# Performance work log

Hardware: AMD Instinct MI355X
Metric: run time of the kernel (lower is better)

## Reference

```python
import jax, jax.numpy as jnp
import numpy as np
import math

B, L, D = 4, 2048, 768
N_HEADS = 12
CHUNK = 8  # query_mask=1 every CHUNK tokens -> f = B*L/CHUNK, f % B == 0
VOCAB = 50000


def setup_inputs() -> dict:
    key = jax.random.key(0)
    ks = jax.random.split(key, 8)
    scale = 1.0 / math.sqrt(D)
    x_qk = jax.random.normal(ks[0], (B, L, D), jnp.float32)
    x_v = jax.random.normal(ks[1], (B, L, D), jnp.float32)
    # deterministic query mask: feature boundary every CHUNK tokens
    pos = jnp.arange(L)
    query_mask = jnp.tile((pos % CHUNK == 0).astype(jnp.int32)[None, :], (B, 1))
    input_ids = jax.random.randint(ks[2], (B, L), 2, VOCAB).astype(jnp.int64)
    # make the last 16 tokens of each row padding to exercise the pad mask
    input_ids = input_ids.at[:, -16:].set(1)
    Wq = jax.random.normal(ks[3], (D, D), jnp.float32) * scale
    Wk = jax.random.normal(ks[4], (D, D), jnp.float32) * scale
    Wv = jax.random.normal(ks[5], (D, D), jnp.float32) * scale
    Wo = jax.random.normal(ks[6], (D, D), jnp.float32) * scale
    zb = jnp.zeros((D,), jnp.float32)
    return {"x_qk": x_qk, "x_v": x_v, "query_mask": query_mask,
            "input_ids": input_ids, "pad_token_id": 1,
            "Wq": Wq, "bq": zb, "Wk": Wk, "bk": zb,
            "Wv": Wv, "bv": zb, "Wo": Wo, "bo": zb}


def reference(x_qk, x_v, query_mask, input_ids, pad_token_id,
              Wq, bq, Wk, bk, Wv, bv, Wo, bo):
    b, l, d = x_qk.shape
    n = b * l
    qm = query_mask.reshape(-1)
    f = int(np.asarray(jnp.sum(qm)))  # static feature count (f % b == 0)
    idx = jnp.nonzero(qm == 1, size=f)[0]                     # [f] query positions
    # segment boundaries: [left_i, right_i) per feature
    left = idx
    right = jnp.concatenate([idx[1:], jnp.array([n], idx.dtype)])
    pos = jnp.arange(n)
    seg_mask = (pos[None, :] >= left[:, None]) & (pos[None, :] < right[:, None])
    seg_mask = seg_mask & (input_ids.reshape(-1) != pad_token_id)[None, :]  # [f, n]

    xq = x_qk.reshape(n, d)
    xv = x_v.reshape(n, d)
    query = xq[idx]                                           # [f, d]
    q = query @ Wq.T + bq                                     # [f, d]
    k = xq @ Wk.T + bk                                        # [n, d]
    v = xv @ Wv.T + bv                                        # [n, d]

    dh = d // N_HEADS
    qh = q.reshape(f, N_HEADS, dh).transpose(1, 0, 2)         # [h, f, dh]
    kh = k.reshape(n, N_HEADS, dh).transpose(1, 0, 2)         # [h, n, dh]
    vh = v.reshape(n, N_HEADS, dh).transpose(1, 0, 2)         # [h, n, dh]

    bias = (1.0 - seg_mask.astype(jnp.float32)) * -10000.0    # [f, n]
    scores = jnp.einsum('hfd,hnd->hfn', qh, kh) / math.sqrt(dh) + bias[None]
    attn = jax.nn.softmax(scores, axis=-1)                    # [h, f, n]
    out = jnp.einsum('hfn,hnd->hfd', attn, vh)                # [h, f, dh]
    out = out.transpose(1, 0, 2).reshape(f, d)
    out = out @ Wo.T + bo
    return out.reshape(b, f // b, d)
```

## Files before the change

### kernel.cpp

```cpp
#include <hip/hip_runtime.h>

#define DMODEL 768
#define NHEADS 12
#define MAXFULL 16

typedef __attribute__((ext_vector_type(8))) short short8;
typedef __attribute__((ext_vector_type(4))) float f32x4;

__device__ __forceinline__ unsigned pack2_bf16(float a, float b) {
  unsigned ua = __float_as_uint(a), ub = __float_as_uint(b);
  ua = (ua + 0x7fffu + ((ua >> 16) & 1u)) >> 16;
  ub = (ub + 0x7fffu + ((ub >> 16) & 1u)) & 0xffff0000u;
  return ua | ub;
}
__device__ __forceinline__ unsigned short bf16_1(float a) {
  unsigned ua = __float_as_uint(a);
  return (unsigned short)((ua + 0x7fffu + ((ua >> 16) & 1u)) >> 16);
}

__device__ __forceinline__ void load16_lds(const void* g, void* l) {
  __builtin_amdgcn_global_load_lds(
      (const __attribute__((address_space(1))) unsigned int*)g,
      (__attribute__((address_space(3))) unsigned int*)l, 16, 0, 0);
}

__global__ __launch_bounds__(256) void convW(const float* __restrict__ w0,
    const float* __restrict__ w1, const float* __restrict__ w2,
    const float* __restrict__ w3, unsigned* __restrict__ o0,
    unsigned* __restrict__ o1, unsigned* __restrict__ o2,
    unsigned* __restrict__ o3, int count) {
  const int nv = count >> 2;
  const float* src[4] = {w0, w1, w2, w3};
  unsigned* dst[4] = {o0, o1, o2, o3};
  for (int idx = blockIdx.x * 256 + threadIdx.x; idx < 4 * nv;
       idx += gridDim.x * 256) {
    int m = idx / nv, r = idx - m * nv;
    float4 v = ((const float4*)src[m])[r];
    dst[m][2 * r]     = pack2_bf16(v.x, v.y);
    dst[m][2 * r + 1] = pack2_bf16(v.z, v.w);
  }
}

__global__ __launch_bounds__(256) void convX(const float* __restrict__ x0,
    const float* __restrict__ x1, unsigned* __restrict__ o0,
    unsigned* __restrict__ o1, int count) {
  const int nv = count >> 2;
  for (int idx = blockIdx.x * 256 + threadIdx.x; idx < 2 * nv;
       idx += gridDim.x * 256) {
    int m = idx / nv, r = idx - m * nv;
    float4 v = m ? ((const float4*)x1)[r] : ((const float4*)x0)[r];
    unsigned* d = m ? o1 : o0;
    d[2 * r]     = pack2_bf16(v.x, v.y);
    d[2 * r + 1] = pack2_bf16(v.z, v.w);
  }
}

struct GSeg {
  const unsigned short* A;
  const unsigned short* W;
  const float* bias;
  const int* row_map;
  float* C;
  int base;
};

__global__ __launch_bounds__(256) void gemm128(GSeg g0, GSeg g1, GSeg g2) {
  __shared__ __attribute__((aligned(16))) unsigned short As[128 * 32];
  __shared__ __attribute__((aligned(16))) unsigned short Bs[128 * 32];
  const int t = threadIdx.x;
  const int id = blockIdx.x;
  const GSeg& d = (id >= g2.base) ? g2 : ((id >= g1.base) ? g1 : g0);
  const int lid = id - d.base;
  const int xcd = lid & 7, j = lid >> 3;
  const int bn = (j % 6) * 128;
  const int bm = ((j / 6) * 8 + xcd) * 128;
  const int lane = t & 63, wid = t >> 6;
  const int m16 = lane & 15, quad = lane >> 4;
  const int wm = (wid >> 1) * 64, wn = (wid & 1) * 64;

  f32x4 acc[4][4];
#pragma unroll
  for (int i = 0; i < 4; ++i)
#pragma unroll
    for (int j2 = 0; j2 < 4; ++j2) acc[i][j2] = (f32x4){0.f, 0.f, 0.f, 0.f};

  const int srow = wid * 32 + (lane >> 2);
  const int skc = (lane & 3) * 8;
  int arow0, arow1;
  if (d.row_map) {
    arow0 = d.row_map[bm + srow];
    arow1 = d.row_map[bm + srow + 16];
  } else {
    arow0 = bm + srow;
    arow1 = bm + srow + 16;
  }
  const int wrow0 = bn + srow, wrow1 = bn + srow + 16;
  unsigned short* As0 = &As[(wid * 32) * 32];
  unsigned short* As1 = &As[(wid * 32 + 16) * 32];
  unsigned short* Bs0 = &Bs[(wid * 32) * 32];
  unsigned short* Bs1 = &Bs[(wid * 32 + 16) * 32];

  for (int k0 = 0; k0 < DMODEL; k0 += 32) {
    load16_lds(d.A + (size_t)arow0 * DMODEL + k0 + skc, As0);
    load16_lds(d.A + (size_t)arow1 * DMODEL + k0 + skc, As1);
    load16_lds(d.W + (size_t)wrow0 * DMODEL + k0 + skc, Bs0);
    load16_lds(d.W + (size_t)wrow1 * DMODEL + k0 + skc, Bs1);
    __syncthreads();
    short8 a[4], b[4];
#pragma unroll
    for (int i = 0; i < 4; ++i)
      a[i] = *(const short8*)&As[(wm + i * 16 + m16) * 32 + quad * 8];
#pragma unroll
    for (int j2 = 0; j2 < 4; ++j2)
      b[j2] = *(const short8*)&Bs[(wn + j2 * 16 + m16) * 32 + quad * 8];
#pragma unroll
    for (int i = 0; i < 4; ++i)
#pragma unroll
      for (int j2 = 0; j2 < 4; ++j2)
        acc[i][j2] = __builtin_amdgcn_mfma_f32_16x16x32_bf16(a[i], b[j2], acc[i][j2], 0, 0, 0);
    __syncthreads();
  }

  float bv[4]; int bcol[4];
#pragma unroll
  for (int j2 = 0; j2 < 4; ++j2) {
    bcol[j2] = bn + wn + j2 * 16 + m16;
    bv[j2] = d.bias[bcol[j2]];
  }
#pragma unroll
  for (int i = 0; i < 4; ++i) {
    const int rbase = bm + wm + i * 16 + quad * 4;
#pragma unroll
    for (int r = 0; r < 4; ++r) {
      const int row = rbase + r;
#pragma unroll
      for (int j2 = 0; j2 < 4; ++j2)
        d.C[(size_t)row * DMODEL + bcol[j2]] = acc[i][j2][r] + bv[j2];
    }
  }
}

__global__ __launch_bounds__(1024) void build_segments(const int* __restrict__ qm,
    const int* __restrict__ ids, const int* __restrict__ padp,
    int n, int f, int* __restrict__ left, int* __restrict__ right,
    int* __restrict__ nvalid, int* __restrict__ fullrank,
    int* __restrict__ fullist, int* __restrict__ nfull) {
  __shared__ int cnt[1024];
  __shared__ int fullcnt;
  const int t = threadIdx.x;
  if (t == 0) fullcnt = 0;
  const int per = (n + 1023) >> 10;
  const int base = t * per;
  int c = 0;
  for (int i = 0; i < per; ++i) {
    int p = base + i;
    if (p < n && qm[p] != 0) ++c;
  }
  cnt[t] = c;
  __syncthreads();
  for (int off = 1; off < 1024; off <<= 1) {
    int v = (t >= off) ? cnt[t - off] : 0;
    __syncthreads();
    cnt[t] += v;
    __syncthreads();
  }
  int r = cnt[t] - c;
  for (int i = 0; i < per; ++i) {
    int p = base + i;
    if (p < n && qm[p] != 0) {
      if (r < f) left[r] = p;
      ++r;
    }
  }
  __syncthreads();
  const int pad = *padp;
  for (int i = t; i < f; i += 1024) {
    int L0 = left[i];
    int R0 = (i + 1 < f) ? left[i + 1] : n;
    right[i] = R0;
    int cv = 0;
    for (int p = L0; p < R0; ++p) cv += (ids[p] != pad) ? 1 : 0;
    nvalid[i] = cv;
    if (cv == 0) {
      int rk = atomicAdd(&fullcnt, 1);
      if (rk < MAXFULL) { fullist[rk] = i; fullrank[i] = rk; }
      else fullrank[i] = -1;
    } else {
      fullrank[i] = -1;
    }
  }
  __syncthreads();
  if (t == 0) *nfull = (fullcnt < MAXFULL) ? fullcnt : MAXFULL;
}

__device__ __forceinline__ float allreduce64(float x) {
#pragma unroll
  for (int m = 1; m < 64; m <<= 1) x += __shfl_xor(x, m, 64);
  return x;
}

__global__ __launch_bounds__(64) void attn_seg(const float* __restrict__ q,
    const float* __restrict__ k, const float* __restrict__ v,
    const int* __restrict__ left, const int* __restrict__ right,
    const int* __restrict__ nvalid, const int* __restrict__ ids,
    const int* __restrict__ padp, unsigned short* __restrict__ out) {
  const int feat = blockIdx.x, h = blockIdx.y, lane = threadIdx.x;
  if (nvalid[feat] == 0) return;
  const int off = h * 64 + lane;
  const int pad = *padp;
  const float qv = q[(size_t)feat * DMODEL + off];
  float m = -1e30f, l = 0.f, acc = 0.f;
  const int L0 = left[feat], R0 = right[feat];
  for (int p = L0; p < R0; ++p) {
    if (ids[p] == pad) continue;
    float s = allreduce64(qv * k[(size_t)p * DMODEL + off]) * 0.125f;
    float mn = fmaxf(m, s);
    float al = __expf(m - mn);
    float w = __expf(s - mn);
    l = l * al + w;
    acc = acc * al + w * v[(size_t)p * DMODEL + off];
    m = mn;
  }
  out[(size_t)feat * DMODEL + off] = bf16_1(acc / l);
}

__global__ __launch_bounds__(256) void attn_full_part(const float* __restrict__ q,
    const float* __restrict__ k, const float* __restrict__ v,
    const int* __restrict__ fullist, const int* __restrict__ nfullp,
    int n, int P, float* __restrict__ pm, float* __restrict__ pl,
    float* __restrict__ pacc) {
  const int nfull = *nfullp;
  if (nfull == 0) return;
  const int t = threadIdx.x, lane = t & 63, wv = t >> 6;
  const int gw = blockIdx.x * 4 + wv;
  const int h = gw / P, piece = gw - h * P;
  const int pk = n / P;

  __shared__ float q_lds[8 * 64];
  __shared__ float w_lds[4][64 * 8];

  for (int idx = t; idx < 8 * 64; idx += 256) {
    int fl = idx >> 6, d = idx & 63;
    q_lds[idx] = (fl < nfull) ? q[(size_t)fullist[fl] * DMODEL + h * 64 + d] : 0.f;
  }
  __syncthreads();

  float m[8], l[8], acc[8];
#pragma unroll
  for (int f_ = 0; f_ < 8; ++f_) { m[f_] = -1e30f; l[f_] = 0.f; acc[f_] = 0.f; }

  for (int c = 0; c < pk; c += 64) {
    const int pc = piece * pk + c;
    float s[8];
#pragma unroll
    for (int f_ = 0; f_ < 8; ++f_) s[f_] = 0.f;
    const float4* kp = (const float4*)(k + (size_t)(pc + lane) * DMODEL + h * 64);
#pragma unroll 1
    for (int g = 0; g < 2; ++g) {
      float4 kv0 = kp[g * 8 + 0], kv1 = kp[g * 8 + 1], kv2 = kp[g * 8 + 2],
             kv3 = kp[g * 8 + 3], kv4 = kp[g * 8 + 4], kv5 = kp[g * 8 + 5],
             kv6 = kp[g * 8 + 6], kv7 = kp[g * 8 + 7];
      const float4* qb = (const float4*)&q_lds[g * 32];
#pragma unroll
      for (int f_ = 0; f_ < 8; ++f_) {
        float4 q0 = qb[f_ * 16 + 0], q1 = qb[f_ * 16 + 1], q2 = qb[f_ * 16 + 2],
               q3 = qb[f_ * 16 + 3], q4 = qb[f_ * 16 + 4], q5 = qb[f_ * 16 + 5],
               q6 = qb[f_ * 16 + 6], q7 = qb[f_ * 16 + 7];
        float acc0 = q0.x * kv0.x + q0.y * kv0.y + q0.z * kv0.z + q0.w * kv0.w;
        acc0 += q1.x * kv1.x + q1.y * kv1.y + q1.z * kv1.z + q1.w * kv1.w;
        acc0 += q2.x * kv2.x + q2.y * kv2.y + q2.z * kv2.z + q2.w * kv2.w;
        acc0 += q3.x * kv3.x + q3.y * kv3.y + q3.z * kv3.z + q3.w * kv3.w;
        acc0 += q4.x * kv4.x + q4.y * kv4.y + q4.z * kv4.z + q4.w * kv4.w;
        acc0 += q5.x * kv5.x + q5.y * kv5.y + q5.z * kv5.z + q5.w * kv5.w;
        acc0 += q6.x * kv6.x + q6.y * kv6.y + q6.z * kv6.z + q6.w * kv6.w;
        acc0 += q7.x * kv7.x + q7.y * kv7.y + q7.z * kv7.z + q7.w * kv7.w;
        s[f_] += acc0;
      }
    }
    float mx[8];
#pragma unroll
    for (int f_ = 0; f_ < 8; ++f_) mx[f_] = s[f_] * 0.125f;
#pragma unroll
    for (int f_ = 0; f_ < 8; ++f_) s[f_] = mx[f_];
#pragma unroll
    for (int st = 1; st < 64; st <<= 1)
#pragma unroll
      for (int f_ = 0; f_ < 8; ++f_) mx[f_] = fmaxf(mx[f_], __shfl_xor(mx[f_], st, 64));
    float alpha[8], w[8], sum[8];
#pragma unroll
    for (int f_ = 0; f_ < 8; ++f_) {
      float mn = fmaxf(m[f_], mx[f_]);
      alpha[f_] = __expf(m[f_] - mn);
      w[f_] = __expf(s[f_] - mn);
      m[f_] = mn;
      sum[f_] = w[f_];
    }
#pragma unroll
    for (int st = 1; st < 64; st <<= 1)
#pragma unroll
      for (int f_ = 0; f_ < 8; ++f_) sum[f_] += __shfl_xor(sum[f_], st, 64);
#pragma unroll
    for (int f_ = 0; f_ < 8; ++f_) l[f_] = l[f_] * alpha[f_] + sum[f_];
    *(float4*)&w_lds[wv][lane * 8]     = make_float4(w[0], w[1], w[2], w[3]);
    *(float4*)&w_lds[wv][lane * 8 + 4] = make_float4(w[4], w[5], w[6], w[7]);
#pragma unroll
    for (int f_ = 0; f_ < 8; ++f_) acc[f_] *= alpha[f_];
    const float* vb = v + (size_t)pc * DMODEL + h * 64 + lane;
#pragma unroll 4
    for (int kk = 0; kk < 64; ++kk) {
      float vd = vb[(size_t)kk * DMODEL];
      float4 wa = *(const float4*)&w_lds[wv][kk * 8];
      float4 wb = *(const float4*)&w_lds[wv][kk * 8 + 4];
      acc[0] += wa.x * vd; acc[1] += wa.y * vd; acc[2] += wa.z * vd; acc[3] += wa.w * vd;
      acc[4] += wb.x * vd; acc[5] += wb.y * vd; acc[6] += wb.z * vd; acc[7] += wb.w * vd;
    }
  }

  for (int f_ = 0; f_ < nfull; ++f_) {
    size_t idx = ((size_t)f_ * NHEADS + h) * P + piece;
    if (lane == 0) { pm[idx] = m[f_]; pl[idx] = l[f_]; }
    pacc[idx * 64 + lane] = acc[f_];
  }
}

__global__ __launch_bounds__(256) void attn_full_comb(
    const int* __restrict__ fullist, const int* __restrict__ nfullp,
    int P, const float* __restrict__ pm, const float* __restrict__ pl,
    const float* __restrict__ pacc, unsigned short* __restrict__ out) {
  const int fl = blockIdx.x, h = blockIdx.y;
  if (fl >= *nfullp) return;
  const int feat = fullist[fl];
  const int t = threadIdx.x, lane = t & 63, wv = t >> 6;
  const size_t base = ((size_t)fl * NHEADS + h) * P;

  __shared__ float s_pm[128];
  __shared__ float s_sc[128];
  __shared__ float s_red[4];
  __shared__ float s_part[4][64];

  for (int sp = t; sp < P; sp += 256) s_pm[sp] = pm[base + sp];
  __syncthreads();
  float mloc = -1e30f;
  for (int sp = t; sp < P; sp += 256) mloc = fmaxf(mloc, s_pm[sp]);
#pragma unroll
  for (int st = 1; st < 64; st <<= 1) mloc = fmaxf(mloc, __shfl_xor(mloc, st, 64));
  if (lane == 0) s_red[wv] = mloc;
  __syncthreads();
  const float M = fmaxf(fmaxf(s_red[0], s_red[1]), fmaxf(s_red[2], s_red[3]));
  __syncthreads();
  float lloc = 0.f;
  for (int sp = t; sp < P; sp += 256) {
    float sc = __expf(s_pm[sp] - M);
    s_sc[sp] = sc;
    lloc += pl[base + sp] * sc;
  }
#pragma unroll
  for (int st = 1; st < 64; st <<= 1) lloc += __shfl_xor(lloc, st, 64);
  if (lane == 0) s_red[wv] = lloc;
  __syncthreads();
  const float Lt = s_red[0] + s_red[1] + s_red[2] + s_red[3];
  float At = 0.f;
  for (int sp = wv; sp < P; sp += 4)
    At += pacc[(base + sp) * 64 + lane] * s_sc[sp];
  s_part[wv][lane] = At;
  __syncthreads();
  if (wv == 0) {
    float tot = s_part[0][lane] + s_part[1][lane] + s_part[2][lane] + s_part[3][lane];
    out[(size_t)feat * DMODEL + h * 64 + lane] = bf16_1(tot / Lt);
  }
}

extern "C" void kernel_launch(void* const* d_in, const int* in_sizes, int n_in,
                              void* d_out, int out_size, void* d_ws, size_t ws_size,
                              hipStream_t stream) {
  const float* x_qk = (const float*)d_in[0];
  const float* x_v  = (const float*)d_in[1];
  const int* qm     = (const int*)d_in[2];
  const int* ids    = (const int*)d_in[3];
  const int* padp   = (const int*)d_in[4];
  const float* Wq = (const float*)d_in[5];
  const float* bq = (const float*)d_in[6];
  const float* Wk = (const float*)d_in[7];
  const float* bk = (const float*)d_in[8];
  const float* Wv = (const float*)d_in[9];
  const float* bv = (const float*)d_in[10];
  const float* Wo = (const float*)d_in[11];
  const float* bo = (const float*)d_in[12];

  const int n = in_sizes[0] / DMODEL;
  const int f = out_size / DMODEL;

  float* kf = (float*)d_ws;
  float* vf = kf + (size_t)n * DMODEL;
  float* qf = vf + (size_t)n * DMODEL;
  unsigned short* af = (unsigned short*)(qf + (size_t)f * DMODEL);
  unsigned short* wqb = af + (size_t)f * DMODEL;
  unsigned short* wkb = wqb + DMODEL * DMODEL;
  unsigned short* wvb = wkb + DMODEL * DMODEL;
  unsigned short* wob = wvb + DMODEL * DMODEL;
  unsigned short* xqb = wob + DMODEL * DMODEL;
  unsigned short* xvb = xqb + (size_t)n * DMODEL;
  int* left     = (int*)(xvb + (size_t)n * DMODEL);
  int* right    = left + f;
  int* nvalid   = right + f;
  int* fullrank = nvalid + f;
  int* fullist  = fullrank + f;
  int* nfull    = fullist + MAXFULL;
  size_t off_bytes = ((size_t)((char*)(nfull + 1) - (char*)d_ws) + 255) & ~(size_t)255;
  int P = 128;
  while (P > 16) {
    size_t need = (size_t)MAXFULL * NHEADS * P * 66 * sizeof(float);
    if (off_bytes + need <= ws_size && (n / P) % 64 == 0 && n % P == 0) break;
    P >>= 1;
  }
  float* pm = (float*)((char*)d_ws + off_bytes);
  float* pl = pm + (size_t)MAXFULL * NHEADS * P;
  float* pacc = pl + (size_t)MAXFULL * NHEADS * P;

  build_segments<<<1, 1024, 0, stream>>>(qm, ids, padp, n, f, left, right,
                                         nvalid, fullrank, fullist, nfull);
  convW<<<1152, 256, 0, stream>>>(Wq, Wk, Wv, Wo, (unsigned*)wqb, (unsigned*)wkb,
                                  (unsigned*)wvb, (unsigned*)wob, DMODEL * DMODEL);
  convX<<<2048, 256, 0, stream>>>(x_qk, x_v, (unsigned*)xqb, (unsigned*)xvb,
                                  n * DMODEL);

  const int TKV = 6 * (n / 128);
  const int TF  = 6 * (f / 128);
  GSeg g0 = { xqb, wkb, bk, nullptr, kf, 0 };
  GSeg g1 = { xvb, wvb, bv, nullptr, vf, TKV };
  GSeg g2 = { xqb, wqb, bq, left,    qf, 2 * TKV };
  gemm128<<<2 * TKV + TF, 256, 0, stream>>>(g0, g1, g2);

  attn_seg<<<dim3(f, NHEADS), 64, 0, stream>>>(qf, kf, vf, left, right, nvalid,
                                               ids, padp, af);
  attn_full_part<<<NHEADS * P / 4, 256, 0, stream>>>(qf, kf, vf, fullist, nfull,
                                                     n, P, pm, pl, pacc);
  attn_full_comb<<<dim3(MAXFULL, NHEADS), 256, 0, stream>>>(fullist, nfull, P,
                                                            pm, pl, pacc, af);

  GSeg gout = { af, wob, bo, nullptr, (float*)d_out, 0 };
  GSeg gnull = { af, wob, bo, nullptr, (float*)d_out, 1 << 30 };
  gemm128<<<TF, 256, 0, stream>>>(gout, gnull, gnull);
}
```

Measured before the change: 233.0 us.

## Triple-buffer GEMM LDS loads and pack four features per attn_seg block

Rewrites the bf16 MFMA GEMM main loop into a three-stage LDS ring. Loads for future K-steps are issued ahead and waited on with explicit vmcnt counts and raw barriers, so global-to-LDS traffic overlaps MFMA compute. LDS use triples, and correctness now depends on the hand-counted waitcnt values. Separately, attn_seg now runs four features per 256-thread block instead of one 64-thread block per feature, cutting the block count; this assumes f is divisible by 4.

```diff
diff --git a/kernel.cpp b/kernel.cpp
--- a/kernel.cpp
+++ b/kernel.cpp
@@ -3,6 +3,7 @@
 #define DMODEL 768
 #define NHEADS 12
 #define MAXFULL 16
+#define NSTEP 24
 
 typedef __attribute__((ext_vector_type(8))) short short8;
 typedef __attribute__((ext_vector_type(4))) float f32x4;
@@ -64,9 +65,35 @@
   int base;
 };
 
+__device__ __forceinline__ void stage_step(const GSeg& d, int k0, int arow0,
+    int arow1, int wrow0, int wrow1, int skc, unsigned short* AsB,
+    unsigned short* BsB, int woff) {
+  load16_lds(d.A + (size_t)arow0 * DMODEL + k0 + skc, AsB + woff);
+  load16_lds(d.A + (size_t)arow1 * DMODEL + k0 + skc, AsB + woff + 16 * 32);
+  load16_lds(d.W + (size_t)wrow0 * DMODEL + k0 + skc, BsB + woff);
+  load16_lds(d.W + (size_t)wrow1 * DMODEL + k0 + skc, BsB + woff + 16 * 32);
+}
+
+__device__ __forceinline__ void compute_step(const unsigned short* AsB,
+    const unsigned short* BsB, int wm, int wn, int m16, int quad,
+    f32x4 acc[4][4]) {
+  short8 a[4], b[4];
+#pragma unroll
+  for (int i = 0; i < 4; ++i)
+    a[i] = *(const short8*)&AsB[(wm + i * 16 + m16) * 32 + quad * 8];
+#pragma unroll
+  for (int j2 = 0; j2 < 4; ++j2)
+    b[j2] = *(const short8*)&BsB[(wn + j2 * 16 + m16) * 32 + quad * 8];
+#pragma unroll
+  for (int i = 0; i < 4; ++i)
+#pragma unroll
+    for (int j2 = 0; j2 < 4; ++j2)
+      acc[i][j2] = __builtin_amdgcn_mfma_f32_16x16x32_bf16(a[i], b[j2], acc[i][j2], 0, 0, 0);
+}
+
 __global__ __launch_bounds__(256) void gemm128(GSeg g0, GSeg g1, GSeg g2) {
-  __shared__ __attribute__((aligned(16))) unsigned short As[128 * 32];
-  __shared__ __attribute__((aligned(16))) unsigned short Bs[128 * 32];
+  __shared__ __attribute__((aligned(16))) unsigned short As[3][128 * 32];
+  __shared__ __attribute__((aligned(16))) unsigned short Bs[3][128 * 32];
   const int t = threadIdx.x;
   const int id = blockIdx.x;
   const GSeg& d = (id >= g2.base) ? g2 : ((id >= g1.base) ? g1 : g0);
@@ -95,31 +122,40 @@
     arow1 = bm + srow + 16;
   }
   const int wrow0 = bn + srow, wrow1 = bn + srow + 16;
-  unsigned short* As0 = &As[(wid * 32) * 32];
-  unsigned short* As1 = &As[(wid * 32 + 16) * 32];
-  unsigned short* Bs0 = &Bs[(wid * 32) * 32];
-  unsigned short* Bs1 = &Bs[(wid * 32 + 16) * 32];
-
-  for (int k0 = 0; k0 < DMODEL; k0 += 32) {
-    load16_lds(d.A + (size_t)arow0 * DMODEL + k0 + skc, As0);
-    load16_lds(d.A + (size_t)arow1 * DMODEL + k0 + skc, As1);
-    load16_lds(d.W + (size_t)wrow0 * DMODEL + k0 + skc, Bs0);
-    load16_lds(d.W + (size_t)wrow1 * DMODEL + k0 + skc, Bs1);
-    __syncthreads();
-    short8 a[4], b[4];
-#pragma unroll
-    for (int i = 0; i < 4; ++i)
-      a[i] = *(const short8*)&As[(wm + i * 16 + m16) * 32 + quad * 8];
-#pragma unroll
-    for (int j2 = 0; j2 < 4; ++j2)
-      b[j2] = *(const short8*)&Bs[(wn + j2 * 16 + m16) * 32 + quad * 8];
-#pragma unroll
-    for (int i = 0; i < 4; ++i)
-#pragma unroll
-      for (int j2 = 0; j2 < 4; ++j2)
-        acc[i][j2] = __builtin_amdgcn_mfma_f32_16x16x32_bf16(a[i], b[j2], acc[i][j2], 0, 0, 0);
-    __syncthreads();
-  }
+  const int woff = (wid * 32) * 32;
+
+  stage_step(d, 0,  arow0, arow1, wrow0, wrow1, skc, &As[0][0], &Bs[0][0], woff);
+  stage_step(d, 32, arow0, arow1, wrow0, wrow1, skc, &As[1][0], &Bs[1][0], woff);
+  stage_step(d, 64, arow0, arow1, wrow0, wrow1, skc, &As[2][0], &Bs[2][0], woff);
+
+#pragma unroll 1
+  for (int g = 0; g < (NSTEP - 3) / 3; ++g) {
+    const int t0 = g * 3;
+#pragma unroll
+    for (int u = 0; u < 3; ++u) {
+      const int ts = t0 + u;
+      asm volatile("s_waitcnt vmcnt(8)" ::: "memory");
+      __builtin_amdgcn_s_barrier();
+      __builtin_amdgcn_sched_barrier(0);
+      compute_step(&As[u][0], &Bs[u][0], wm, wn, m16, quad, acc);
+      __builtin_amdgcn_s_barrier();
+      __builtin_amdgcn_sched_barrier(0);
+      stage_step(d, (ts + 3) * 32, arow0, arow1, wrow0, wrow1, skc,
+                 &As[u][0], &Bs[u][0], woff);
+    }
+  }
+  asm volatile("s_waitcnt vmcnt(8)" ::: "memory");
+  __builtin_amdgcn_s_barrier();
+  __builtin_amdgcn_sched_barrier(0);
+  compute_step(&As[0][0], &Bs[0][0], wm, wn, m16, quad, acc);
+  asm volatile("s_waitcnt vmcnt(4)" ::: "memory");
+  __builtin_amdgcn_s_barrier();
+  __builtin_amdgcn_sched_barrier(0);
+  compute_step(&As[1][0], &Bs[1][0], wm, wn, m16, quad, acc);
+  asm volatile("s_waitcnt vmcnt(0)" ::: "memory");
+  __builtin_amdgcn_s_barrier();
+  __builtin_amdgcn_sched_barrier(0);
+  compute_step(&As[2][0], &Bs[2][0], wm, wn, m16, quad, acc);
 
   float bv[4]; int bcol[4];
 #pragma unroll
@@ -199,12 +235,13 @@
   return x;
 }
 
-__global__ __launch_bounds__(64) void attn_seg(const float* __restrict__ q,
+__global__ __launch_bounds__(256) void attn_seg(const float* __restrict__ q,
     const float* __restrict__ k, const float* __restrict__ v,
     const int* __restrict__ left, const int* __restrict__ right,
     const int* __restrict__ nvalid, const int* __restrict__ ids,
     const int* __restrict__ padp, unsigned short* __restrict__ out) {
-  const int feat = blockIdx.x, h = blockIdx.y, lane = threadIdx.x;
+  const int wid = threadIdx.x >> 6, lane = threadIdx.x & 63;
+  const int feat = blockIdx.x * 4 + wid, h = blockIdx.y;
   if (nvalid[feat] == 0) return;
   const int off = h * 64 + lane;
   const int pad = *padp;
@@ -431,8 +468,8 @@
   GSeg g2 = { xqb, wqb, bq, left,    qf, 2 * TKV };
   gemm128<<<2 * TKV + TF, 256, 0, stream>>>(g0, g1, g2);
 
-  attn_seg<<<dim3(f, NHEADS), 64, 0, stream>>>(qf, kf, vf, left, right, nvalid,
-                                               ids, padp, af);
+  attn_seg<<<dim3(f / 4, NHEADS), 256, 0, stream>>>(qf, kf, vf, left, right,
+                                                    nvalid, ids, padp, af);
   attn_full_part<<<NHEADS * P / 4, 256, 0, stream>>>(qf, kf, vf, fullist, nfull,
                                                      n, P, pm, pl, pacc);
   attn_full_comb<<<dim3(MAXFULL, NHEADS), 256, 0, stream>>>(fullist, nfull, P,
```

Measured after the change: 232.3 us. About the same (-0.3%).
